# Kernel optimization log

Measured on AMD Instinct MI355X. Metric: run time of the kernel, lower is better.

## Reference

```python
import jax, jax.numpy as jnp
import numpy as np

E, MAX_M, K, N = 8, 2048, 2048, 8192

def setup_inputs() -> dict:
    key = jax.random.key(0)
    k1, k2, k3 = jax.random.split(key, 3)
    x_padded = jax.random.normal(k1, (E, MAX_M, K), dtype=jnp.float32)
    stacked_weights = jax.random.normal(k2, (E, N, K), dtype=jnp.float32) * 0.02
    m_sizes = jax.random.randint(k3, (E,), 0, MAX_M, dtype=jnp.int32)
    return {"x_padded": x_padded, "stacked_weights": stacked_weights, "m_sizes": m_sizes}

def reference(x_padded, stacked_weights, m_sizes):
    # valid-token mask per expert: [E, MAX_M]
    mask = (jnp.arange(MAX_M, dtype=jnp.int32)[None, :] < m_sizes[:, None])
    # zero padded rows (pad_expert_inputs fills with zeros)
    x = jnp.where(mask[:, :, None], x_padded, jnp.zeros((), x_padded.dtype))
    # grouped GEMM via batched matmul: [E, M, K] x [E, N, K]^T -> [E, M, N]
    out = jnp.einsum('emk,enk->emn', x, stacked_weights)
    # rows beyond m_sizes[i] are sliced away in the original; mask them to zero
    return jnp.where(mask[:, :, None], out, jnp.zeros((), out.dtype))
```

## Files before the change

kernel.cpp:

```cpp
#include <hip/hip_runtime.h>
#include <hip/hip_bf16.h>


#define NE   8
#define MAXM 2048
#define KD   2048
#define ND   8192

#define BM   256
#define BN   256
#define BK   64
#define NTS  (KD/BK)

typedef __attribute__((ext_vector_type(8))) short          short8;
typedef __attribute__((ext_vector_type(8))) unsigned short us8;
typedef __attribute__((ext_vector_type(4))) float          f32x4;
typedef __attribute__((ext_vector_type(4))) unsigned short us4;

__device__ __forceinline__ unsigned short f2bf(float f) {
    union { float f; unsigned u; } v; v.f = f;
    unsigned u = v.u;
    return (unsigned short)((u + 0x7FFFu + ((u >> 16) & 1u)) >> 16);
}

__device__ __forceinline__ void gload16(const void* g, void* l) {
    __builtin_amdgcn_global_load_lds(
        (const __attribute__((address_space(1))) void*)g,
        (__attribute__((address_space(3))) void*)l, 16, 0, 0);
}

__global__ __launch_bounds__(256) void cvt_kernel(const float* __restrict__ src,
                                                  unsigned short* __restrict__ dst,
                                                  int n8) {
    int i = blockIdx.x * blockDim.x + threadIdx.x;
    int stride = gridDim.x * blockDim.x;
    for (; i < n8; i += stride) {
        const f32x4* s = (const f32x4*)(src + (size_t)i * 8);
        f32x4 a = s[0], b = s[1];
        us8 v = (us8){f2bf(a[0]), f2bf(a[1]), f2bf(a[2]), f2bf(a[3]),
                      f2bf(b[0]), f2bf(b[1]), f2bf(b[2]), f2bf(b[3])};
        *(us8*)(dst + (size_t)i * 8) = v;
    }
}

__global__ __launch_bounds__(256) void cvt_x_kernel(const float* __restrict__ src,
                                                    unsigned short* __restrict__ dst,
                                                    const int* __restrict__ ms) {
    int bid = blockIdx.x;
    int e = bid >> 11, m = bid & 2047;
    if (m >= ms[e]) return;
    const float* s = src + ((size_t)e * MAXM + m) * KD;
    unsigned short* d = dst + ((size_t)e * MAXM + m) * KD;
    int t = threadIdx.x;
    const f32x4* s4 = (const f32x4*)(s + t * 8);
    f32x4 a = s4[0], b = s4[1];
    us8 v = (us8){f2bf(a[0]), f2bf(a[1]), f2bf(a[2]), f2bf(a[3]),
                  f2bf(b[0]), f2bf(b[1]), f2bf(b[2]), f2bf(b[3])};
    *(us8*)(d + t * 8) = v;
}

__global__ __launch_bounds__(512, 2) void ggemm_pers(
    const unsigned short* __restrict__ xb,
    const unsigned short* __restrict__ wb,
    const int*   __restrict__ ms,
    float*       __restrict__ out)
{
    int p   = blockIdx.x;
    int xcd = p & 7;
    int jj  = p >> 3;
    int tid = threadIdx.x;

    __shared__ int s_live[8], s_dead[8], s_cnt[2];
    __shared__ unsigned short Ak[2][2][BM * 32];
    __shared__ unsigned short Bk[2][2][BN * 32];

    if (tid == 0) {
        int nl = 0, nd = 0, cumL = 0, cumD = 0, il = jj, id = jj;
        #pragma unroll
        for (int e = 0; e < NE; ++e) {
            int L = (ms[e] + 255) >> 8;
            int cntL = L << 2, cntD = (8 - L) << 2;
            while (il < cumL + cntL) { int o = il - cumL; s_live[nl++] = (e << 5) | ((o >> 2) << 2) | (o & 3); il += 32; }
            while (id < cumD + cntD) { int o = id - cumD; s_dead[nd++] = (e << 5) | ((L + (o >> 2)) << 2) | (o & 3); id += 32; }
            cumL += cntL; cumD += cntD;
        }
        s_cnt[0] = nl; s_cnt[1] = nd;
    }
    __syncthreads();

    int ndead = s_cnt[1];
    #pragma unroll 1
    for (int d = 0; d < ndead; ++d) {
        int v = s_dead[d]; int e = v >> 5, br = (v >> 2) & 7, bcl = v & 3;
        float* outE = out + (size_t)e * MAXM * ND;
        int row0 = br * BM, col0 = (xcd * 4 + bcl) * BN;
        f32x4 z = (f32x4){0.f, 0.f, 0.f, 0.f};
        #pragma unroll
        for (int q = 0; q < 32; ++q) {
            int i2 = tid + q * 512;
            int rr = i2 >> 6, cc = (i2 & 63) << 2;
            *(f32x4*)(outE + (size_t)(row0 + rr) * ND + col0 + cc) = z;
        }
    }
    int nlive = s_cnt[0];
    if (nlive == 0) return;

    int wid = tid >> 6, lane = tid & 63;
    int wr = wid >> 2, wc = wid & 3;
    int lr = lane & 15, kg = lane >> 4;
    int srow = lane >> 2;
    int ss   = (lane & 3) ^ ((lane >> 3) & 3);

    auto stageA = [&](int b, int kh, const unsigned short* xP, int kt) {
        #pragma unroll
        for (int q = 0; q < 2; ++q) {
            int blk = wid * 2 + q;
            const unsigned short* src =
                xP + (size_t)(blk * 16 + srow) * KD + kt * BK + kh * 32 + ss * 8;
            gload16(src, (char*)&Ak[b][kh][0] + blk * 1024);
        }
    };
    auto stageB = [&](int b, int kh, const unsigned short* wP, int kt) {
        #pragma unroll
        for (int q = 0; q < 2; ++q) {
            int blk = wid * 2 + q;
            const unsigned short* src =
                wP + (size_t)(blk * 16 + srow) * KD + kt * BK + kh * 32 + ss * 8;
            gload16(src, (char*)&Bk[b][kh][0] + blk * 1024);
        }
    };

    f32x4 acc[8][4];
    #pragma unroll
    for (int mf = 0; mf < 8; ++mf)
        #pragma unroll
        for (int nf = 0; nf < 4; ++nf)
            acc[mf][nf] = (f32x4){0.f, 0.f, 0.f, 0.f};

    const unsigned short *xC, *wC, *xN, *wN;
    float *oC, *oN;
    int msC, r0C, c0C, msN, r0N, c0N;
    {
        int v = s_live[0]; int e = v >> 5, br = (v >> 2) & 7, bcl = v & 3;
        r0C = br * BM; c0C = (xcd * 4 + bcl) * BN; msC = ms[e];
        xC = xb + ((size_t)e * MAXM + r0C) * KD;
        wC = wb + ((size_t)e * ND + c0C) * KD;
        oC = out + (size_t)e * MAXM * ND;
    }
    if (nlive > 1) {
        int v = s_live[1]; int e = v >> 5, br = (v >> 2) & 7, bcl = v & 3;
        r0N = br * BM; c0N = (xcd * 4 + bcl) * BN; msN = ms[e];
        xN = xb + ((size_t)e * MAXM + r0N) * KD;
        wN = wb + ((size_t)e * ND + c0N) * KD;
        oN = out + (size_t)e * MAXM * ND;
    } else { xN = xC; wN = wC; oN = oC; msN = msC; r0N = r0C; c0N = c0C; }

    stageA(0, 0, xC, 0); stageB(0, 0, wC, 0);
    stageA(0, 1, xC, 0); stageB(0, 1, wC, 0);

    #pragma unroll 1
    for (int s = 0; s < nlive; ++s) {
        bool last  = (s + 1 >= nlive);
        bool alive = (r0C + wr * 128) < msC;

        auto phase = [&](int b, int kh, bool vm4, bool stg,
                         const unsigned short* xS, const unsigned short* wS, int kts) {
            if (vm4) { asm volatile("s_waitcnt vmcnt(4)" ::: "memory"); }
            else     { asm volatile("s_waitcnt vmcnt(0)" ::: "memory"); }
            __builtin_amdgcn_s_barrier();
            if (stg) { stageA(b ^ 1, kh, xS, kts); stageB(b ^ 1, kh, wS, kts); }
            if (alive) {
                short8 a[8], bf[4];
                #pragma unroll
                for (int i = 0; i < 4; ++i) {
                    int row  = wc * 64 + i * 16 + lr;
                    int slot = kg ^ ((row >> 1) & 3);
                    bf[i] = *(const short8*)&Bk[b][kh][row * 32 + slot * 8];
                }
                #pragma unroll
                for (int mf = 0; mf < 8; ++mf) {
                    int row  = wr * 128 + mf * 16 + lr;
                    int slot = kg ^ ((row >> 1) & 3);
                    a[mf] = *(const short8*)&Ak[b][kh][row * 32 + slot * 8];
                }
                #pragma unroll
                for (int mf = 0; mf < 8; ++mf)
                    #pragma unroll
                    for (int nf = 0; nf < 4; ++nf)
                        acc[mf][nf] = __builtin_amdgcn_mfma_f32_16x16x32_bf16(a[mf], bf[nf], acc[mf][nf], 0, 0, 0);
            }
        };

        #pragma unroll 1
        for (int kt = 0; kt < NTS; ++kt) {
            int b = kt & 1;
            bool has_next = (kt + 1 < NTS) || (!last);
            const unsigned short* xS = (kt + 1 < NTS) ? xC : xN;
            const unsigned short* wS = (kt + 1 < NTS) ? wC : wN;
            int kts = (kt + 1 < NTS) ? kt + 1 : 0;
            phase(b, 0, true, has_next, xS, wS, kts);
            phase(b, 1, has_next, has_next, xS, wS, kts);
        }

        #pragma unroll
        for (int mf = 0; mf < 8; ++mf) {
            int rbase = r0C + wr * 128 + mf * 16 + kg * 4;
            #pragma unroll
            for (int nf = 0; nf < 4; ++nf) {
                int gc = c0C + wc * 64 + nf * 16 + lr;
                #pragma unroll
                for (int q = 0; q < 4; ++q) {
                    int gr = rbase + q;
                    float v = (gr < msC) ? acc[mf][nf][q] : 0.f;
                    oC[(size_t)gr * ND + gc] = v;
                    acc[mf][nf][q] = 0.f;
                }
            }
        }

        xC = xN; wC = wN; oC = oN; msC = msN; r0C = r0N; c0C = c0N;
        if (s + 2 < nlive) {
            int v = s_live[s + 2]; int e = v >> 5, br = (v >> 2) & 7, bcl = v & 3;
            r0N = br * BM; c0N = (xcd * 4 + bcl) * BN; msN = ms[e];
            xN = xb + ((size_t)e * MAXM + r0N) * KD;
            wN = wb + ((size_t)e * ND + c0N) * KD;
            oN = out + (size_t)e * MAXM * ND;
        }
    }
}

#define FBM 128
#define FBK 32
#define FTM (MAXM/FBM)
#define FTN (ND/FBM)
#define FNT (KD/FBK)
#define LSTR 40
__global__ __launch_bounds__(256, 2) void ggemm_fused(
    const float* __restrict__ x, const float* __restrict__ w,
    const int* __restrict__ ms, float* __restrict__ out)
{
    int nwg  = gridDim.x;
    int orig = blockIdx.x;
    int cpx  = nwg >> 3;
    int bid  = (orig & 7) * cpx + (orig >> 3);
    int e   = bid / (FTM * FTN);
    int rem = bid % (FTM * FTN);
    int br  = rem % FTM;
    int bc  = rem / FTM;
    int m_size = ms[e];
    int row0 = br * FBM, col0 = bc * FBM;
    float* outE = out + (size_t)e * MAXM * ND;
    int tid = threadIdx.x;

    if (row0 >= m_size) {
        f32x4 z = (f32x4){0.f, 0.f, 0.f, 0.f};
        #pragma unroll
        for (int q = 0; q < 16; ++q) {
            int i2 = tid + q * 256;
            int rr = i2 >> 5, cc = (i2 & 31) << 2;
            *(f32x4*)(outE + (size_t)(row0 + rr) * ND + col0 + cc) = z;
        }
        return;
    }

    const float* xE = x + ((size_t)e * MAXM + row0) * KD;
    const float* wE = w + ((size_t)e * ND   + col0) * KD;

    __shared__ unsigned short As[2][FBM][LSTR];
    __shared__ unsigned short Bs[2][FBM][LSTR];

    int sr  = tid >> 3;
    int sc4 = tid & 7;
    int wid = tid >> 6, lane = tid & 63;
    int wr = wid >> 1, wc = wid & 1;
    int lr = lane & 15, kg = lane >> 4;

    f32x4 acc[4][4];
    #pragma unroll
    for (int m = 0; m < 4; ++m)
        #pragma unroll
        for (int n = 0; n < 4; ++n)
            acc[m][n] = (f32x4){0.f, 0.f, 0.f, 0.f};

    {
        #pragma unroll
        for (int q = 0; q < 4; ++q) {
            int r0 = sr + q * 32;
            f32x4 av = *(const f32x4*)(xE + (size_t)r0 * KD + sc4 * 4);
            f32x4 bv = *(const f32x4*)(wE + (size_t)r0 * KD + sc4 * 4);
            us4 ah = (us4){f2bf(av[0]), f2bf(av[1]), f2bf(av[2]), f2bf(av[3])};
            us4 bh = (us4){f2bf(bv[0]), f2bf(bv[1]), f2bf(bv[2]), f2bf(bv[3])};
            *(us4*)&As[0][r0][sc4 * 4] = ah;
            *(us4*)&Bs[0][r0][sc4 * 4] = bh;
        }
    }
    __syncthreads();

    for (int t = 0; t < FNT; ++t) {
        int cur = t & 1;
        f32x4 av[4], bv[4];
        bool pre = (t + 1 < FNT);
        if (pre) {
            const float* xk = xE + (size_t)(t + 1) * FBK;
            const float* wk = wE + (size_t)(t + 1) * FBK;
            #pragma unroll
            for (int q = 0; q < 4; ++q) {
                int r0 = sr + q * 32;
                av[q] = *(const f32x4*)(xk + (size_t)r0 * KD + sc4 * 4);
                bv[q] = *(const f32x4*)(wk + (size_t)r0 * KD + sc4 * 4);
            }
        }
        short8 a[4], b[4];
        #pragma unroll
        for (int m = 0; m < 4; ++m)
            a[m] = *(const short8*)&As[cur][wr * 64 + m * 16 + lr][kg * 8];
        #pragma unroll
        for (int n = 0; n < 4; ++n)
            b[n] = *(const short8*)&Bs[cur][wc * 64 + n * 16 + lr][kg * 8];
        #pragma unroll
        for (int m = 0; m < 4; ++m)
            #pragma unroll
            for (int n = 0; n < 4; ++n)
                acc[m][n] = __builtin_amdgcn_mfma_f32_16x16x32_bf16(a[m], b[n], acc[m][n], 0, 0, 0);

        if (pre) {
            int nb = cur ^ 1;
            #pragma unroll
            for (int q = 0; q < 4; ++q) {
                int r0 = sr + q * 32;
                us4 ah = (us4){f2bf(av[q][0]), f2bf(av[q][1]), f2bf(av[q][2]), f2bf(av[q][3])};
                us4 bh = (us4){f2bf(bv[q][0]), f2bf(bv[q][1]), f2bf(bv[q][2]), f2bf(bv[q][3])};
                *(us4*)&As[nb][r0][sc4 * 4] = ah;
                *(us4*)&Bs[nb][r0][sc4 * 4] = bh;
            }
        }
        __syncthreads();
    }

    #pragma unroll
    for (int m = 0; m < 4; ++m) {
        int rbase = row0 + wr * 64 + m * 16 + kg * 4;
        #pragma unroll
        for (int n = 0; n < 4; ++n) {
            int gc = col0 + wc * 64 + n * 16 + lr;
            #pragma unroll
            for (int q = 0; q < 4; ++q) {
                int gr = rbase + q;
                float v = (gr < m_size) ? acc[m][n][q] : 0.f;
                outE[(size_t)gr * ND + gc] = v;
            }
        }
    }
}

extern "C" void kernel_launch(void* const* d_in, const int* in_sizes, int n_in,
                              void* d_out, int out_size, void* d_ws, size_t ws_size,
                              hipStream_t stream) {
    const float* x  = (const float*)d_in[0];
    const float* w  = (const float*)d_in[1];
    const int*   ms = (const int*)d_in[2];
    float* out = (float*)d_out;

    const size_t xElems = (size_t)NE * MAXM * KD;
    const size_t wElems = (size_t)NE * ND   * KD;
    const size_t need   = (xElems + wElems) * 2;

    if (ws_size >= need) {
        unsigned short* xb = (unsigned short*)d_ws;
        unsigned short* wb = xb + xElems;
        cvt_x_kernel<<<NE * MAXM, 256, 0, stream>>>(x, xb, ms);
        cvt_kernel<<<2048, 256, 0, stream>>>(w, wb, (int)(wElems / 8));
        ggemm_pers<<<256, 512, 0, stream>>>(xb, wb, ms, out);
    } else {
        ggemm_fused<<<dim3(NE * (MAXM/FBM) * (ND/FBM)), dim3(256), 0, stream>>>(x, w, ms, out);
    }
}
```

Before: 663.1 us.

## Split K-tile into four interleaved LDS-read/stage/MFMA phases with priority boosts

After: 604.8 us. -8.8%, faster.

```diff
diff --git a/kernel.cpp b/kernel.cpp
--- a/kernel.cpp
+++ b/kernel.cpp
@@ -157,49 +157,131 @@
 
     stageA(0, 0, xC, 0); stageB(0, 0, wC, 0);
     stageA(0, 1, xC, 0); stageB(0, 1, wC, 0);
+    asm volatile("s_waitcnt vmcnt(4)" ::: "memory");
+    __builtin_amdgcn_s_barrier();
 
     #pragma unroll 1
     for (int s = 0; s < nlive; ++s) {
         bool last  = (s + 1 >= nlive);
         bool alive = (r0C + wr * 128) < msC;
 
-        auto phase = [&](int b, int kh, bool vm4, bool stg,
-                         const unsigned short* xS, const unsigned short* wS, int kts) {
-            if (vm4) { asm volatile("s_waitcnt vmcnt(4)" ::: "memory"); }
-            else     { asm volatile("s_waitcnt vmcnt(0)" ::: "memory"); }
-            __builtin_amdgcn_s_barrier();
-            if (stg) { stageA(b ^ 1, kh, xS, kts); stageB(b ^ 1, kh, wS, kts); }
-            if (alive) {
-                short8 a[8], bf[4];
-                #pragma unroll
-                for (int i = 0; i < 4; ++i) {
-                    int row  = wc * 64 + i * 16 + lr;
-                    int slot = kg ^ ((row >> 1) & 3);
-                    bf[i] = *(const short8*)&Bk[b][kh][row * 32 + slot * 8];
-                }
-                #pragma unroll
-                for (int mf = 0; mf < 8; ++mf) {
-                    int row  = wr * 128 + mf * 16 + lr;
-                    int slot = kg ^ ((row >> 1) & 3);
-                    a[mf] = *(const short8*)&Ak[b][kh][row * 32 + slot * 8];
-                }
-                #pragma unroll
-                for (int mf = 0; mf < 8; ++mf)
-                    #pragma unroll
-                    for (int nf = 0; nf < 4; ++nf)
-                        acc[mf][nf] = __builtin_amdgcn_mfma_f32_16x16x32_bf16(a[mf], bf[nf], acc[mf][nf], 0, 0, 0);
-            }
-        };
-
         #pragma unroll 1
         for (int kt = 0; kt < NTS; ++kt) {
             int b = kt & 1;
-            bool has_next = (kt + 1 < NTS) || (!last);
+            bool stg = (kt + 1 < NTS) || (!last);
             const unsigned short* xS = (kt + 1 < NTS) ? xC : xN;
             const unsigned short* wS = (kt + 1 < NTS) ? wC : wN;
             int kts = (kt + 1 < NTS) ? kt + 1 : 0;
-            phase(b, 0, true, has_next, xS, wS, kts);
-            phase(b, 1, has_next, has_next, xS, wS, kts);
+
+            short8 a[4], bf[4];
+
+            if (alive) {
+                #pragma unroll
+                for (int i = 0; i < 4; ++i) {
+                    int row  = wc * 64 + i * 16 + lr;
+                    int slot = kg ^ ((row >> 1) & 3);
+                    bf[i] = *(const short8*)&Bk[b][0][row * 32 + slot * 8];
+                }
+                #pragma unroll
+                for (int i = 0; i < 4; ++i) {
+                    int row  = wr * 128 + i * 16 + lr;
+                    int slot = kg ^ ((row >> 1) & 3);
+                    a[i] = *(const short8*)&Ak[b][0][row * 32 + slot * 8];
+                }
+            }
+            if (stg) stageA(b ^ 1, 0, xS, kts);
+            __builtin_amdgcn_s_barrier();
+            asm volatile("s_waitcnt lgkmcnt(0)" ::: "memory");
+            __builtin_amdgcn_sched_barrier(0);
+            __builtin_amdgcn_s_setprio(1);
+            if (alive) {
+                #pragma unroll
+                for (int i = 0; i < 4; ++i)
+                    #pragma unroll
+                    for (int nf = 0; nf < 4; ++nf)
+                        acc[i][nf] = __builtin_amdgcn_mfma_f32_16x16x32_bf16(a[i], bf[nf], acc[i][nf], 0, 0, 0);
+            }
+            __builtin_amdgcn_s_setprio(0);
+            __builtin_amdgcn_s_barrier();
+
+            if (alive) {
+                #pragma unroll
+                for (int i = 0; i < 4; ++i) {
+                    int row  = wr * 128 + 64 + i * 16 + lr;
+                    int slot = kg ^ ((row >> 1) & 3);
+                    a[i] = *(const short8*)&Ak[b][0][row * 32 + slot * 8];
+                }
+            }
+            if (stg) stageB(b ^ 1, 0, wS, kts);
+            __builtin_amdgcn_s_barrier();
+            asm volatile("s_waitcnt lgkmcnt(0)" ::: "memory");
+            __builtin_amdgcn_sched_barrier(0);
+            __builtin_amdgcn_s_setprio(1);
+            if (alive) {
+                #pragma unroll
+                for (int i = 0; i < 4; ++i)
+                    #pragma unroll
+                    for (int nf = 0; nf < 4; ++nf)
+                        acc[4 + i][nf] = __builtin_amdgcn_mfma_f32_16x16x32_bf16(a[i], bf[nf], acc[4 + i][nf], 0, 0, 0);
+            }
+            __builtin_amdgcn_s_setprio(0);
+            if (stg) { asm volatile("s_waitcnt vmcnt(4)" ::: "memory"); }
+            else     { asm volatile("s_waitcnt vmcnt(0)" ::: "memory"); }
+            __builtin_amdgcn_s_barrier();
+
+            if (alive) {
+                #pragma unroll
+                for (int i = 0; i < 4; ++i) {
+                    int row  = wc * 64 + i * 16 + lr;
+                    int slot = kg ^ ((row >> 1) & 3);
+                    bf[i] = *(const short8*)&Bk[b][1][row * 32 + slot * 8];
+                }
+                #pragma unroll
+                for (int i = 0; i < 4; ++i) {
+                    int row  = wr * 128 + i * 16 + lr;
+                    int slot = kg ^ ((row >> 1) & 3);
+                    a[i] = *(const short8*)&Ak[b][1][row * 32 + slot * 8];
+                }
+            }
+            if (stg) stageA(b ^ 1, 1, xS, kts);
+            __builtin_amdgcn_s_barrier();
+            asm volatile("s_waitcnt lgkmcnt(0)" ::: "memory");
+            __builtin_amdgcn_sched_barrier(0);
+            __builtin_amdgcn_s_setprio(1);
+            if (alive) {
+                #pragma unroll
+                for (int i = 0; i < 4; ++i)
+                    #pragma unroll
+                    for (int nf = 0; nf < 4; ++nf)
+                        acc[i][nf] = __builtin_amdgcn_mfma_f32_16x16x32_bf16(a[i], bf[nf], acc[i][nf], 0, 0, 0);
+            }
+            __builtin_amdgcn_s_setprio(0);
+            __builtin_amdgcn_s_barrier();
+
+            if (alive) {
+                #pragma unroll
+                for (int i = 0; i < 4; ++i) {
+                    int row  = wr * 128 + 64 + i * 16 + lr;
+                    int slot = kg ^ ((row >> 1) & 3);
+                    a[i] = *(const short8*)&Ak[b][1][row * 32 + slot * 8];
+                }
+            }
+            if (stg) stageB(b ^ 1, 1, wS, kts);
+            __builtin_amdgcn_s_barrier();
+            asm volatile("s_waitcnt lgkmcnt(0)" ::: "memory");
+            __builtin_amdgcn_sched_barrier(0);
+            __builtin_amdgcn_s_setprio(1);
+            if (alive) {
+                #pragma unroll
+                for (int i = 0; i < 4; ++i)
+                    #pragma unroll
+                    for (int nf = 0; nf < 4; ++nf)
+                        acc[4 + i][nf] = __builtin_amdgcn_mfma_f32_16x16x32_bf16(a[i], bf[nf], acc[4 + i][nf], 0, 0, 0);
+            }
+            __builtin_amdgcn_s_setprio(0);
+            if (stg) { asm volatile("s_waitcnt vmcnt(4)" ::: "memory"); }
+            else     { asm volatile("s_waitcnt vmcnt(0)" ::: "memory"); }
+            __builtin_amdgcn_s_barrier();
         }
 
         #pragma unroll
```

## Fuse weight bf16 conversion into GEMM with fp32 LDS staging and triple buffering

Applied to the files above, without the earlier changes.

Result: faster. 631.7 us (-4.7%).

```diff
diff --git a/kernel.cpp b/kernel.cpp
--- a/kernel.cpp
+++ b/kernel.cpp
@@ -9,7 +9,7 @@
 
 #define BM   256
 #define BN   256
-#define BK   64
+#define BK   32
 #define NTS  (KD/BK)
 
 typedef __attribute__((ext_vector_type(8))) short          short8;
@@ -27,20 +27,6 @@
     __builtin_amdgcn_global_load_lds(
         (const __attribute__((address_space(1))) void*)g,
         (__attribute__((address_space(3))) void*)l, 16, 0, 0);
-}
-
-__global__ __launch_bounds__(256) void cvt_kernel(const float* __restrict__ src,
-                                                  unsigned short* __restrict__ dst,
-                                                  int n8) {
-    int i = blockIdx.x * blockDim.x + threadIdx.x;
-    int stride = gridDim.x * blockDim.x;
-    for (; i < n8; i += stride) {
-        const f32x4* s = (const f32x4*)(src + (size_t)i * 8);
-        f32x4 a = s[0], b = s[1];
-        us8 v = (us8){f2bf(a[0]), f2bf(a[1]), f2bf(a[2]), f2bf(a[3]),
-                      f2bf(b[0]), f2bf(b[1]), f2bf(b[2]), f2bf(b[3])};
-        *(us8*)(dst + (size_t)i * 8) = v;
-    }
 }
 
 __global__ __launch_bounds__(256) void cvt_x_kernel(const float* __restrict__ src,
@@ -61,7 +47,7 @@
 
 __global__ __launch_bounds__(512, 2) void ggemm_pers(
     const unsigned short* __restrict__ xb,
-    const unsigned short* __restrict__ wb,
+    const float*          __restrict__ w,
     const int*   __restrict__ ms,
     float*       __restrict__ out)
 {
@@ -71,8 +57,8 @@
     int tid = threadIdx.x;
 
     __shared__ int s_live[8], s_dead[8], s_cnt[2];
-    __shared__ unsigned short Ak[2][2][BM * 32];
-    __shared__ unsigned short Bk[2][2][BN * 32];
+    __shared__ unsigned short Ak[3][BM * 32];
+    __shared__ float          Bk[3][BN * 32];
 
     if (tid == 0) {
         int nl = 0, nd = 0, cumL = 0, cumD = 0, il = jj, id = jj;
@@ -110,23 +96,51 @@
     int lr = lane & 15, kg = lane >> 4;
     int srow = lane >> 2;
     int ss   = (lane & 3) ^ ((lane >> 3) & 3);
-
-    auto stageA = [&](int b, int kh, const unsigned short* xP, int kt) {
+    int brow = lane >> 3;
+    int ssb  = (lane & 7) ^ ((lane >> 3) & 7);
+
+    auto stageA = [&](int r, const unsigned short* xP, int kt) {
         #pragma unroll
         for (int q = 0; q < 2; ++q) {
             int blk = wid * 2 + q;
             const unsigned short* src =
-                xP + (size_t)(blk * 16 + srow) * KD + kt * BK + kh * 32 + ss * 8;
-            gload16(src, (char*)&Ak[b][kh][0] + blk * 1024);
+                xP + (size_t)(blk * 16 + srow) * KD + kt * BK + ss * 8;
+            gload16(src, (char*)&Ak[r][0] + blk * 1024);
         }
     };
-    auto stageB = [&](int b, int kh, const unsigned short* wP, int kt) {
-        #pragma unroll
-        for (int q = 0; q < 2; ++q) {
-            int blk = wid * 2 + q;
-            const unsigned short* src =
-                wP + (size_t)(blk * 16 + srow) * KD + kt * BK + kh * 32 + ss * 8;
-            gload16(src, (char*)&Bk[b][kh][0] + blk * 1024);
+    auto stageBf = [&](int r, const float* wP, int kt) {
+        #pragma unroll
+        for (int q = 0; q < 4; ++q) {
+            int blk = wid * 4 + q;
+            const float* src =
+                wP + (size_t)(blk * 8 + brow) * KD + kt * BK + ssb * 4;
+            gload16(src, (char*)&Bk[r][0] + blk * 1024);
+        }
+    };
+    auto ldA = [&](short8* a, int r) {
+        #pragma unroll
+        for (int mf = 0; mf < 8; ++mf) {
+            int row  = wr * 128 + mf * 16 + lr;
+            int slot = kg ^ ((row >> 1) & 3);
+            a[mf] = *(const short8*)&Ak[r][row * 32 + slot * 8];
+        }
+    };
+    auto ldB4f = [&](short8* bfr, int r) {
+        #pragma unroll
+        for (int i = 0; i < 4; ++i) {
+            int row = wc * 64 + i * 16 + lr;
+            int s0  = (kg * 2)     ^ (row & 7);
+            int s1  = (kg * 2 + 1) ^ (row & 7);
+            f32x4 lo = *(const f32x4*)&Bk[r][row * 32 + s0 * 4];
+            f32x4 hi = *(const f32x4*)&Bk[r][row * 32 + s1 * 4];
+            unsigned u0, u1, u2, u3;
+            asm("v_cvt_pk_bf16_f32 %0, %1, %2" : "=v"(u0) : "v"(lo[0]), "v"(lo[1]));
+            asm("v_cvt_pk_bf16_f32 %0, %1, %2" : "=v"(u1) : "v"(lo[2]), "v"(lo[3]));
+            asm("v_cvt_pk_bf16_f32 %0, %1, %2" : "=v"(u2) : "v"(hi[0]), "v"(hi[1]));
+            asm("v_cvt_pk_bf16_f32 %0, %1, %2" : "=v"(u3) : "v"(hi[2]), "v"(hi[3]));
+            union { unsigned u[4]; short8 s; } pk;
+            pk.u[0] = u0; pk.u[1] = u1; pk.u[2] = u2; pk.u[3] = u3;
+            bfr[i] = pk.s;
         }
     };
 
@@ -137,69 +151,62 @@
         for (int nf = 0; nf < 4; ++nf)
             acc[mf][nf] = (f32x4){0.f, 0.f, 0.f, 0.f};
 
-    const unsigned short *xC, *wC, *xN, *wN;
+    const unsigned short *xC, *xN;
+    const float *wC, *wN;
     float *oC, *oN;
     int msC, r0C, c0C, msN, r0N, c0N;
     {
         int v = s_live[0]; int e = v >> 5, br = (v >> 2) & 7, bcl = v & 3;
         r0C = br * BM; c0C = (xcd * 4 + bcl) * BN; msC = ms[e];
         xC = xb + ((size_t)e * MAXM + r0C) * KD;
-        wC = wb + ((size_t)e * ND + c0C) * KD;
+        wC = w  + ((size_t)e * ND + c0C) * KD;
         oC = out + (size_t)e * MAXM * ND;
     }
     if (nlive > 1) {
         int v = s_live[1]; int e = v >> 5, br = (v >> 2) & 7, bcl = v & 3;
         r0N = br * BM; c0N = (xcd * 4 + bcl) * BN; msN = ms[e];
         xN = xb + ((size_t)e * MAXM + r0N) * KD;
-        wN = wb + ((size_t)e * ND + c0N) * KD;
+        wN = w  + ((size_t)e * ND + c0N) * KD;
         oN = out + (size_t)e * MAXM * ND;
     } else { xN = xC; wN = wC; oN = oC; msN = msC; r0N = r0C; c0N = c0C; }
 
-    stageA(0, 0, xC, 0); stageB(0, 0, wC, 0);
-    stageA(0, 1, xC, 0); stageB(0, 1, wC, 0);
+    stageA(0, xC, 0); stageBf(0, wC, 0);
+    stageA(1, xC, 1); stageBf(1, wC, 1);
+    asm volatile("s_waitcnt vmcnt(6)" ::: "memory");
+    __builtin_amdgcn_s_barrier();
+
+    int cur = 0;
 
     #pragma unroll 1
     for (int s = 0; s < nlive; ++s) {
         bool last  = (s + 1 >= nlive);
         bool alive = (r0C + wr * 128) < msC;
 
-        auto phase = [&](int b, int kh, bool vm4, bool stg,
-                         const unsigned short* xS, const unsigned short* wS, int kts) {
-            if (vm4) { asm volatile("s_waitcnt vmcnt(4)" ::: "memory"); }
-            else     { asm volatile("s_waitcnt vmcnt(0)" ::: "memory"); }
+        #pragma unroll 1
+        for (int kt = 0; kt < NTS; ++kt) {
+            bool stg = (kt + 2 < NTS) || (!last);
+            const unsigned short* xS = (kt + 2 < NTS) ? xC : xN;
+            const float*          wS = (kt + 2 < NTS) ? wC : wN;
+            int k2 = (kt + 2 < NTS) ? kt + 2 : kt + 2 - NTS;
+            int rs = (cur >= 1) ? cur - 1 : 2;
+
+            if (stg) { stageA(rs, xS, k2); stageBf(rs, wS, k2); }
+            short8 a[8], bfr[4];
+            if (alive) { ldB4f(bfr, cur); ldA(a, cur); }
             __builtin_amdgcn_s_barrier();
-            if (stg) { stageA(b ^ 1, kh, xS, kts); stageB(b ^ 1, kh, wS, kts); }
+            __builtin_amdgcn_s_setprio(1);
             if (alive) {
-                short8 a[8], bf[4];
-                #pragma unroll
-                for (int i = 0; i < 4; ++i) {
-                    int row  = wc * 64 + i * 16 + lr;
-                    int slot = kg ^ ((row >> 1) & 3);
-                    bf[i] = *(const short8*)&Bk[b][kh][row * 32 + slot * 8];
-                }
-                #pragma unroll
-                for (int mf = 0; mf < 8; ++mf) {
-                    int row  = wr * 128 + mf * 16 + lr;
-                    int slot = kg ^ ((row >> 1) & 3);
-                    a[mf] = *(const short8*)&Ak[b][kh][row * 32 + slot * 8];
-                }
                 #pragma unroll
                 for (int mf = 0; mf < 8; ++mf)
                     #pragma unroll
                     for (int nf = 0; nf < 4; ++nf)
-                        acc[mf][nf] = __builtin_amdgcn_mfma_f32_16x16x32_bf16(a[mf], bf[nf], acc[mf][nf], 0, 0, 0);
-            }
-        };
-
-        #pragma unroll 1
-        for (int kt = 0; kt < NTS; ++kt) {
-            int b = kt & 1;
-            bool has_next = (kt + 1 < NTS) || (!last);
-            const unsigned short* xS = (kt + 1 < NTS) ? xC : xN;
-            const unsigned short* wS = (kt + 1 < NTS) ? wC : wN;
-            int kts = (kt + 1 < NTS) ? kt + 1 : 0;
-            phase(b, 0, true, has_next, xS, wS, kts);
-            phase(b, 1, has_next, has_next, xS, wS, kts);
+                        acc[mf][nf] = __builtin_amdgcn_mfma_f32_16x16x32_bf16(a[mf], bfr[nf], acc[mf][nf], 0, 0, 0);
+            }
+            __builtin_amdgcn_s_setprio(0);
+            if (stg) { asm volatile("s_waitcnt vmcnt(6)" ::: "memory"); }
+            else     { asm volatile("s_waitcnt vmcnt(0)" ::: "memory"); }
+            __builtin_amdgcn_s_barrier();
+            cur = (cur + 1 == 3) ? 0 : cur + 1;
         }
 
         #pragma unroll
@@ -223,7 +230,7 @@
             int v = s_live[s + 2]; int e = v >> 5, br = (v >> 2) & 7, bcl = v & 3;
             r0N = br * BM; c0N = (xcd * 4 + bcl) * BN; msN = ms[e];
             xN = xb + ((size_t)e * MAXM + r0N) * KD;
-            wN = wb + ((size_t)e * ND + c0N) * KD;
+            wN = w  + ((size_t)e * ND + c0N) * KD;
             oN = out + (size_t)e * MAXM * ND;
         }
     }
@@ -362,15 +369,12 @@
     float* out = (float*)d_out;
 
     const size_t xElems = (size_t)NE * MAXM * KD;
-    const size_t wElems = (size_t)NE * ND   * KD;
-    const size_t need   = (xElems + wElems) * 2;
+    const size_t need   = xElems * 2;
 
     if (ws_size >= need) {
         unsigned short* xb = (unsigned short*)d_ws;
-        unsigned short* wb = xb + xElems;
         cvt_x_kernel<<<NE * MAXM, 256, 0, stream>>>(x, xb, ms);
-        cvt_kernel<<<2048, 256, 0, stream>>>(w, wb, (int)(wElems / 8));
-        ggemm_pers<<<256, 512, 0, stream>>>(xb, wb, ms, out);
+        ggemm_pers<<<256, 512, 0, stream>>>(xb, w, ms, out);
     } else {
         ggemm_fused<<<dim3(NE * (MAXM/FBM) * (ND/FBM)), dim3(256), 0, stream>>>(x, w, ms, out);
     }
```
